# Kernel optimization log

Hardware: AMD Instinct MI355X
Metric: run time of the kernel (lower is better)

## Reference

```python
import jax, jax.numpy as jnp
import numpy as np

N, F_IN, F_OUT = 8192, 256, 256
EDGE_PROB = 0.004  # avg degree ~33


def setup_inputs() -> dict:
    key = jax.random.key(0)
    k1, k2, k3, k4 = jax.random.split(key, 4)
    X = jax.random.normal(k1, (N, F_IN), dtype=jnp.float32)
    # binary adjacency (any nonzero entry in the original is an edge)
    adj = (jax.random.uniform(k2, (N, N)) < EDGE_PROB).astype(jnp.float32)
    W = jax.random.normal(k3, (F_OUT, F_IN), dtype=jnp.float32) * 0.05
    b = jnp.zeros((F_OUT,), dtype=jnp.float32)
    S = jax.random.normal(k4, (2 * F_OUT,), dtype=jnp.float32) * 0.05
    return {"X": X, "adj": adj, "W": W, "b": b, "S": S}


def reference(X, adj, W, b, S):
    # X: [N, F_in], adj: [N, N], W: [F_out, F_in], b: [F_out], S: [2*F_out]
    Xp = X @ W.T + b                      # [N, F_out]
    f = Xp.shape[1]
    n = X.shape[0]
    # per-edge score e_ij = leaky_relu(Xp_i . S[:f] + Xp_j . S[f:])
    a_src = Xp @ S[:f]                    # [N]
    a_dst = Xp @ S[f:]                    # [N]
    e = jax.nn.leaky_relu(a_src[:, None] + a_dst[None, :])  # [N, N]
    # edges = nonzero(adj + I): self-loops always present
    mask = (adj != 0) | jnp.eye(n, dtype=bool)
    e = jnp.where(mask, e, -jnp.inf)
    # local (per-source-node) softmax over neighbors == segment softmax on i
    attn = jax.nn.softmax(e, axis=1)      # [N, N]
    return jax.nn.sigmoid(attn @ Xp)      # [N, F_out]
```

## Files before the change

kernel.cpp:

```cpp
#include <hip/hip_runtime.h>
#include <math.h>

#define NN 8192
#define FF 256
constexpr int BM = 64, BN = 64, BK = 64;
constexpr int MAXN = 256;

__global__ __launch_bounds__(256) void gemm_kernel(const float* __restrict__ X,
                                                   const float* __restrict__ W,
                                                   const float* __restrict__ bias,
                                                   float* __restrict__ Xp) {
    __shared__ float Xs[BK][BM];
    __shared__ float Ws[BK][BN];
    const int tid  = threadIdx.x;
    const int row0 = blockIdx.x * BM;
    const int col0 = blockIdx.y * BN;
    const int ty   = tid >> 4;
    const int tx   = tid & 15;

    const int lrow = tid & 63;
    const int kq0  = (tid >> 6) * 4;

    float acc[4][4] = {};

    for (int kt = 0; kt < FF; kt += BK) {
        __syncthreads();
#pragma unroll
        for (int q = 0; q < 4; ++q) {
            const int kq = kq0 + q;
            const float4 xv = *reinterpret_cast<const float4*>(&X[(row0 + lrow) * FF + kt + kq * 4]);
            const float4 wv = *reinterpret_cast<const float4*>(&W[(col0 + lrow) * FF + kt + kq * 4]);
            Xs[kq * 4 + 0][lrow] = xv.x; Xs[kq * 4 + 1][lrow] = xv.y;
            Xs[kq * 4 + 2][lrow] = xv.z; Xs[kq * 4 + 3][lrow] = xv.w;
            Ws[kq * 4 + 0][lrow] = wv.x; Ws[kq * 4 + 1][lrow] = wv.y;
            Ws[kq * 4 + 2][lrow] = wv.z; Ws[kq * 4 + 3][lrow] = wv.w;
        }
        __syncthreads();
#pragma unroll 8
        for (int k = 0; k < BK; ++k) {
            const float4 a4 = *reinterpret_cast<const float4*>(&Xs[k][ty * 4]);
            const float4 b4 = *reinterpret_cast<const float4*>(&Ws[k][tx * 4]);
            const float av[4] = {a4.x, a4.y, a4.z, a4.w};
            const float bv[4] = {b4.x, b4.y, b4.z, b4.w};
#pragma unroll
            for (int ii = 0; ii < 4; ++ii)
#pragma unroll
                for (int jj = 0; jj < 4; ++jj)
                    acc[ii][jj] = fmaf(av[ii], bv[jj], acc[ii][jj]);
        }
    }

    const float4 b4 = *reinterpret_cast<const float4*>(&bias[col0 + tx * 4]);
#pragma unroll
    for (int ii = 0; ii < 4; ++ii) {
        const int r = row0 + ty * 4 + ii;
        float4 o;
        o.x = acc[ii][0] + b4.x;
        o.y = acc[ii][1] + b4.y;
        o.z = acc[ii][2] + b4.z;
        o.w = acc[ii][3] + b4.w;
        *reinterpret_cast<float4*>(&Xp[(size_t)r * FF + col0 + tx * 4]) = o;
    }
}

__global__ __launch_bounds__(256) void dots_kernel(const float* __restrict__ Xp,
                                                   const float* __restrict__ S,
                                                   float* __restrict__ a_src,
                                                   float* __restrict__ a_dst) {
    const int wid  = threadIdx.x >> 6;
    const int lane = threadIdx.x & 63;
    const int row  = blockIdx.x * 4 + wid;
    const float4 xv = *reinterpret_cast<const float4*>(&Xp[(size_t)row * FF + lane * 4]);
    const float4 s0 = *reinterpret_cast<const float4*>(&S[lane * 4]);
    const float4 s1 = *reinterpret_cast<const float4*>(&S[FF + lane * 4]);
    float ps = xv.x * s0.x + xv.y * s0.y + xv.z * s0.z + xv.w * s0.w;
    float pd = xv.x * s1.x + xv.y * s1.y + xv.z * s1.z + xv.w * s1.w;
#pragma unroll
    for (int off = 32; off; off >>= 1) {
        ps += __shfl_xor(ps, off);
        pd += __shfl_xor(pd, off);
    }
    if (lane == 0) {
        a_src[row] = ps;
        a_dst[row] = pd;
    }
}

__global__ __launch_bounds__(256) void agg_kernel(const float* __restrict__ adj,
                                                  const float* __restrict__ Xp,
                                                  const float* __restrict__ a_src,
                                                  const float* __restrict__ a_dst,
                                                  float* __restrict__ out) {
    __shared__ int   nbr[MAXN];
    __shared__ float wts[MAXN];
    __shared__ float redm[4];
    __shared__ float reds[4];
    __shared__ int   cnt;

    const int i = blockIdx.x;
    const int t = threadIdx.x;
    if (t == 0) cnt = 0;
    __syncthreads();

    const size_t base = (size_t)i * NN;
#pragma unroll
    for (int it = 0; it < NN / (256 * 4); ++it) {
        const int c0 = it * 1024 + t * 4;
        const float4 v = *reinterpret_cast<const float4*>(&adj[base + c0]);
        const float vv[4] = {v.x, v.y, v.z, v.w};
#pragma unroll
        for (int u = 0; u < 4; ++u) {
            const int col = c0 + u;
            if (vv[u] != 0.f || col == i) {
                const int slot = atomicAdd(&cnt, 1);
                if (slot < MAXN) nbr[slot] = col;
            }
        }
    }
    __syncthreads();

    const int n = min(cnt, MAXN);
    const float ai = a_src[i];
    float ev = -INFINITY;
    if (t < n) {
        const float x = ai + a_dst[nbr[t]];
        ev = (x >= 0.f) ? x : 0.01f * x;
    }

    float m = ev;
#pragma unroll
    for (int off = 32; off; off >>= 1) m = fmaxf(m, __shfl_xor(m, off));
    if ((t & 63) == 0) redm[t >> 6] = m;
    __syncthreads();
    m = fmaxf(fmaxf(redm[0], redm[1]), fmaxf(redm[2], redm[3]));

    const float w = (t < n) ? __expf(ev - m) : 0.f;
    wts[t] = w;

    float s = w;
#pragma unroll
    for (int off = 32; off; off >>= 1) s += __shfl_xor(s, off);
    if ((t & 63) == 0) reds[t >> 6] = s;
    __syncthreads();
    const float inv_den = 1.f / (reds[0] + reds[1] + reds[2] + reds[3]);

    float acc = 0.f;
    int k = 0;
    for (; k + 4 <= n; k += 4) {
        const float w0 = wts[k], w1 = wts[k + 1], w2 = wts[k + 2], w3 = wts[k + 3];
        const int j0 = nbr[k], j1 = nbr[k + 1], j2 = nbr[k + 2], j3 = nbr[k + 3];
        acc += w0 * Xp[(size_t)j0 * FF + t] + w1 * Xp[(size_t)j1 * FF + t]
             + w2 * Xp[(size_t)j2 * FF + t] + w3 * Xp[(size_t)j3 * FF + t];
    }
    for (; k < n; ++k) acc += wts[k] * Xp[(size_t)nbr[k] * FF + t];

    const float z = acc * inv_den;
    out[(size_t)i * FF + t] = 1.f / (1.f + __expf(-z));
}

extern "C" void kernel_launch(void* const* d_in, const int* in_sizes, int n_in,
                              void* d_out, int out_size, void* d_ws, size_t ws_size,
                              hipStream_t stream) {
    const float* X   = (const float*)d_in[0];
    const float* adj = (const float*)d_in[1];
    const float* W   = (const float*)d_in[2];
    const float* b   = (const float*)d_in[3];
    const float* S   = (const float*)d_in[4];
    float* out = (float*)d_out;

    float* Xp    = (float*)d_ws;
    float* a_src = Xp + (size_t)NN * FF;
    float* a_dst = a_src + NN;

    gemm_kernel<<<dim3(NN / BM, FF / BN), 256, 0, stream>>>(X, W, b, Xp);
    dots_kernel<<<NN / 4, 256, 0, stream>>>(Xp, S, a_src, a_dst);
    agg_kernel<<<NN, 256, 0, stream>>>(adj, Xp, a_src, a_dst, out);
}
```

Measured before the change: 405.5 us.

## Split aggregation into CSR-build and wave-per-row gather kernels; prefetch GEMM tiles

The fused adjacency-scan/aggregate kernel is split in two. The first kernel scans each adjacency row, computes normalized softmax weights and writes a compact per-row neighbor list to global memory. The second kernel uses one wavefront per output row, gathering neighbor features with float4 loads. The GEMM also register-prefetches the next K tile while computing the current one. MAXN drops to 128, which risks truncating high-degree rows, and the change adds an extra launch plus a global round trip for the neighbor lists.

```diff
diff --git a/kernel.cpp b/kernel.cpp
--- a/kernel.cpp
+++ b/kernel.cpp
@@ -3,41 +3,53 @@
 
 #define NN 8192
 #define FF 256
-constexpr int BM = 64, BN = 64, BK = 64;
-constexpr int MAXN = 256;
+#define MAXN 128
 
 __global__ __launch_bounds__(256) void gemm_kernel(const float* __restrict__ X,
                                                    const float* __restrict__ W,
                                                    const float* __restrict__ bias,
                                                    float* __restrict__ Xp) {
-    __shared__ float Xs[BK][BM];
-    __shared__ float Ws[BK][BN];
+    __shared__ float Xs[64][64];
+    __shared__ float Ws[64][64];
     const int tid  = threadIdx.x;
-    const int row0 = blockIdx.x * BM;
-    const int col0 = blockIdx.y * BN;
+    const int row0 = blockIdx.x * 64;
+    const int col0 = blockIdx.y * 64;
     const int ty   = tid >> 4;
     const int tx   = tid & 15;
-
     const int lrow = tid & 63;
     const int kq0  = (tid >> 6) * 4;
 
+    const float* Xr = &X[(size_t)(row0 + lrow) * FF];
+    const float* Wr = &W[(size_t)(col0 + lrow) * FF];
+
+    float4 px[4], pw[4];
+#pragma unroll
+    for (int q = 0; q < 4; ++q) {
+        px[q] = *reinterpret_cast<const float4*>(&Xr[(kq0 + q) * 4]);
+        pw[q] = *reinterpret_cast<const float4*>(&Wr[(kq0 + q) * 4]);
+    }
+
     float acc[4][4] = {};
 
-    for (int kt = 0; kt < FF; kt += BK) {
+#pragma unroll
+    for (int kt = 0; kt < 4; ++kt) {
+#pragma unroll
+        for (int q = 0; q < 4; ++q) {
+            const int k0 = (kq0 + q) * 4;
+            Xs[k0+0][lrow]=px[q].x; Xs[k0+1][lrow]=px[q].y; Xs[k0+2][lrow]=px[q].z; Xs[k0+3][lrow]=px[q].w;
+            Ws[k0+0][lrow]=pw[q].x; Ws[k0+1][lrow]=pw[q].y; Ws[k0+2][lrow]=pw[q].z; Ws[k0+3][lrow]=pw[q].w;
+        }
         __syncthreads();
-#pragma unroll
-        for (int q = 0; q < 4; ++q) {
-            const int kq = kq0 + q;
-            const float4 xv = *reinterpret_cast<const float4*>(&X[(row0 + lrow) * FF + kt + kq * 4]);
-            const float4 wv = *reinterpret_cast<const float4*>(&W[(col0 + lrow) * FF + kt + kq * 4]);
-            Xs[kq * 4 + 0][lrow] = xv.x; Xs[kq * 4 + 1][lrow] = xv.y;
-            Xs[kq * 4 + 2][lrow] = xv.z; Xs[kq * 4 + 3][lrow] = xv.w;
-            Ws[kq * 4 + 0][lrow] = wv.x; Ws[kq * 4 + 1][lrow] = wv.y;
-            Ws[kq * 4 + 2][lrow] = wv.z; Ws[kq * 4 + 3][lrow] = wv.w;
-        }
-        __syncthreads();
+        if (kt < 3) {
+            const int kb = (kt + 1) * 64;
+#pragma unroll
+            for (int q = 0; q < 4; ++q) {
+                px[q] = *reinterpret_cast<const float4*>(&Xr[kb + (kq0 + q) * 4]);
+                pw[q] = *reinterpret_cast<const float4*>(&Wr[kb + (kq0 + q) * 4]);
+            }
+        }
 #pragma unroll 8
-        for (int k = 0; k < BK; ++k) {
+        for (int k = 0; k < 64; ++k) {
             const float4 a4 = *reinterpret_cast<const float4*>(&Xs[k][ty * 4]);
             const float4 b4 = *reinterpret_cast<const float4*>(&Ws[k][tx * 4]);
             const float av[4] = {a4.x, a4.y, a4.z, a4.w};
@@ -48,6 +60,7 @@
                 for (int jj = 0; jj < 4; ++jj)
                     acc[ii][jj] = fmaf(av[ii], bv[jj], acc[ii][jj]);
         }
+        __syncthreads();
     }
 
     const float4 b4 = *reinterpret_cast<const float4*>(&bias[col0 + tx * 4]);
@@ -86,13 +99,13 @@
     }
 }
 
-__global__ __launch_bounds__(256) void agg_kernel(const float* __restrict__ adj,
-                                                  const float* __restrict__ Xp,
+__global__ __launch_bounds__(256) void csr_kernel(const float* __restrict__ adj,
                                                   const float* __restrict__ a_src,
                                                   const float* __restrict__ a_dst,
-                                                  float* __restrict__ out) {
-    __shared__ int   nbr[MAXN];
-    __shared__ float wts[MAXN];
+                                                  int* __restrict__ cnt_g,
+                                                  int* __restrict__ nbr_g,
+                                                  float* __restrict__ wt_g) {
+    __shared__ int   nbr_s[MAXN];
     __shared__ float redm[4];
     __shared__ float reds[4];
     __shared__ int   cnt;
@@ -104,7 +117,7 @@
 
     const size_t base = (size_t)i * NN;
 #pragma unroll
-    for (int it = 0; it < NN / (256 * 4); ++it) {
+    for (int it = 0; it < NN / 1024; ++it) {
         const int c0 = it * 1024 + t * 4;
         const float4 v = *reinterpret_cast<const float4*>(&adj[base + c0]);
         const float vv[4] = {v.x, v.y, v.z, v.w};
@@ -113,17 +126,19 @@
             const int col = c0 + u;
             if (vv[u] != 0.f || col == i) {
                 const int slot = atomicAdd(&cnt, 1);
-                if (slot < MAXN) nbr[slot] = col;
+                if (slot < MAXN) nbr_s[slot] = col;
             }
         }
     }
     __syncthreads();
 
     const int n = min(cnt, MAXN);
-    const float ai = a_src[i];
+    const float si = a_src[i];
+    int   j  = 0;
     float ev = -INFINITY;
     if (t < n) {
-        const float x = ai + a_dst[nbr[t]];
+        j = nbr_s[t];
+        const float x = si + a_dst[j];
         ev = (x >= 0.f) ? x : 0.01f * x;
     }
 
@@ -135,8 +150,6 @@
     m = fmaxf(fmaxf(redm[0], redm[1]), fmaxf(redm[2], redm[3]));
 
     const float w = (t < n) ? __expf(ev - m) : 0.f;
-    wts[t] = w;
-
     float s = w;
 #pragma unroll
     for (int off = 32; off; off >>= 1) s += __shfl_xor(s, off);
@@ -144,18 +157,62 @@
     __syncthreads();
     const float inv_den = 1.f / (reds[0] + reds[1] + reds[2] + reds[3]);
 
-    float acc = 0.f;
+    if (t < n) {
+        nbr_g[(size_t)i * MAXN + t] = j;
+        wt_g [(size_t)i * MAXN + t] = w * inv_den;
+    }
+    if (t == 0) cnt_g[i] = n;
+}
+
+__global__ __launch_bounds__(256) void agg_kernel(const int* __restrict__ cnt_g,
+                                                  const int* __restrict__ nbr_g,
+                                                  const float* __restrict__ wt_g,
+                                                  const float* __restrict__ Xp,
+                                                  float* __restrict__ out) {
+    __shared__ int   nb[4][MAXN];
+    __shared__ float wt[4][MAXN];
+
+    const int wid  = threadIdx.x >> 6;
+    const int lane = threadIdx.x & 63;
+    const int i    = blockIdx.x * 4 + wid;
+
+    const int n = cnt_g[i];
+    if (lane < n) {
+        nb[wid][lane] = nbr_g[(size_t)i * MAXN + lane];
+        wt[wid][lane] = wt_g [(size_t)i * MAXN + lane];
+    }
+    if (lane + 64 < n) {
+        nb[wid][lane + 64] = nbr_g[(size_t)i * MAXN + lane + 64];
+        wt[wid][lane + 64] = wt_g [(size_t)i * MAXN + lane + 64];
+    }
+    __syncthreads();
+
+    const float* xb = Xp + lane * 4;
+    float4 acc = {0.f, 0.f, 0.f, 0.f};
     int k = 0;
-    for (; k + 4 <= n; k += 4) {
-        const float w0 = wts[k], w1 = wts[k + 1], w2 = wts[k + 2], w3 = wts[k + 3];
-        const int j0 = nbr[k], j1 = nbr[k + 1], j2 = nbr[k + 2], j3 = nbr[k + 3];
-        acc += w0 * Xp[(size_t)j0 * FF + t] + w1 * Xp[(size_t)j1 * FF + t]
-             + w2 * Xp[(size_t)j2 * FF + t] + w3 * Xp[(size_t)j3 * FF + t];
-    }
-    for (; k < n; ++k) acc += wts[k] * Xp[(size_t)nbr[k] * FF + t];
-
-    const float z = acc * inv_den;
-    out[(size_t)i * FF + t] = 1.f / (1.f + __expf(-z));
+    for (; k + 2 <= n; k += 2) {
+        const int   j0 = nb[wid][k],     j1 = nb[wid][k + 1];
+        const float w0 = wt[wid][k],     w1 = wt[wid][k + 1];
+        const float4 v0 = *reinterpret_cast<const float4*>(&xb[(size_t)j0 * FF]);
+        const float4 v1 = *reinterpret_cast<const float4*>(&xb[(size_t)j1 * FF]);
+        acc.x += w0 * v0.x + w1 * v1.x;
+        acc.y += w0 * v0.y + w1 * v1.y;
+        acc.z += w0 * v0.z + w1 * v1.z;
+        acc.w += w0 * v0.w + w1 * v1.w;
+    }
+    if (k < n) {
+        const int   j0 = nb[wid][k];
+        const float w0 = wt[wid][k];
+        const float4 v0 = *reinterpret_cast<const float4*>(&xb[(size_t)j0 * FF]);
+        acc.x += w0 * v0.x; acc.y += w0 * v0.y; acc.z += w0 * v0.z; acc.w += w0 * v0.w;
+    }
+
+    float4 o;
+    o.x = 1.f / (1.f + __expf(-acc.x));
+    o.y = 1.f / (1.f + __expf(-acc.y));
+    o.z = 1.f / (1.f + __expf(-acc.z));
+    o.w = 1.f / (1.f + __expf(-acc.w));
+    *reinterpret_cast<float4*>(&out[(size_t)i * FF + lane * 4]) = o;
 }
 
 extern "C" void kernel_launch(void* const* d_in, const int* in_sizes, int n_in,
@@ -171,8 +228,12 @@
     float* Xp    = (float*)d_ws;
     float* a_src = Xp + (size_t)NN * FF;
     float* a_dst = a_src + NN;
-
-    gemm_kernel<<<dim3(NN / BM, FF / BN), 256, 0, stream>>>(X, W, b, Xp);
+    int*   cnt_g = (int*)(a_dst + NN);
+    int*   nbr_g = cnt_g + NN;
+    float* wt_g  = (float*)(nbr_g + (size_t)NN * MAXN);
+
+    gemm_kernel<<<dim3(NN / 64, FF / 64), 256, 0, stream>>>(X, W, b, Xp);
     dots_kernel<<<NN / 4, 256, 0, stream>>>(Xp, S, a_src, a_dst);
-    agg_kernel<<<NN, 256, 0, stream>>>(adj, Xp, a_src, a_dst, out);
-}
+    csr_kernel<<<NN, 256, 0, stream>>>(adj, a_src, a_dst, cnt_g, nbr_g, wt_g);
+    agg_kernel<<<NN / 4, 256, 0, stream>>>(cnt_g, nbr_g, wt_g, Xp, out);
+}
```

Result: slower. 413.8 us (+2.0%).
